# Kernel tuning notes

Hardware: AMD Instinct MI355X
Metric: run time of the kernel (lower is better)

The kernel has to match this reference:

```python
import jax, jax.numpy as jnp
import numpy as np
import math

DIM_IN = 768
RED = 256
FS = 384


def setup_inputs() -> dict:
    key = jax.random.key(0)
    ks = jax.random.split(key, 20)
    B, Nq, Nk = 16, 1024, FS
    inp = {
        "query_feature": jax.random.normal(ks[0], (B, Nq, DIM_IN), jnp.float32),
        "Input_feature": jax.random.normal(ks[1], (B, Nk, DIM_IN), jnp.float32),
    }
    # six q/k projections: Linear(dim_in -> reduce_dim), torch weight layout [out,in]
    names = ["q1", "q2", "q3", "k1", "k2", "k3"]
    for i, n in enumerate(names):
        inp[f"W{n}"] = 0.01 * jax.random.normal(ks[2 + i], (RED, DIM_IN), jnp.float32)
        inp[f"b{n}"] = jnp.zeros((RED,), jnp.float32)
    # self.layer: Linear(Fs_size -> 1)
    inp["layer_w"] = 0.01 * jax.random.normal(ks[10], (1, FS), jnp.float32)
    inp["layer_b"] = jnp.zeros((1,), jnp.float32)
    # output_layer: Linear(2*dim_in -> dim_in)
    inp["Wout"] = 0.01 * jax.random.normal(ks[11], (DIM_IN, 2 * DIM_IN), jnp.float32)
    inp["bout"] = jnp.zeros((DIM_IN,), jnp.float32)
    return inp


def _proj_center(x, W, b):
    # Linear then subtract per-feature mean over the token axis (dim=1)
    y = jnp.einsum("bnd,rd->bnr", x, W) + b
    return y - y.mean(axis=1, keepdims=True)


def reference(query_feature, Input_feature,
              Wq1, bq1, Wq2, bq2, Wq3, bq3,
              Wk1, bk1, Wk2, bk2, Wk3, bk3,
              layer_w, layer_b, Wout, bout):
    scale = 1.0 / math.sqrt(RED)
    q1 = _proj_center(query_feature, Wq1, bq1)
    q2 = _proj_center(query_feature, Wq2, bq2)
    q3 = _proj_center(query_feature, Wq3, bq3)
    k1 = _proj_center(Input_feature, Wk1, bk1)
    k2 = _proj_center(Input_feature, Wk2, bk2)
    k3 = _proj_center(Input_feature, Wk3, bk3)

    aw1 = jax.nn.softmax(jnp.einsum("bnr,bmr->bnm", q1, q2) * scale, axis=2)  # [B,Nq,Nq]
    aw2 = jax.nn.softmax(jnp.einsum("bnr,bmr->bnm", k1, k2) * scale, axis=2)  # [B,Nk,Nk]
    aw3 = jax.nn.softmax(jnp.einsum("bnr,bmr->bnm", q3, k3) * scale, axis=2)  # [B,Nq,Nk]

    attention_feature1 = jnp.einsum("bnm,bmd->bnd", aw1, query_feature)  # [B,Nq,D]
    hidden = jnp.einsum("bnm,om->bno", aw2, layer_w) + layer_b  # [B,Nk,1]
    hidden = jax.nn.softmax(hidden, axis=1)
    add = aw3 + jnp.swapaxes(hidden, 1, 2)  # broadcast [B,1,Nk]
    attention_feature2 = jnp.einsum("bnm,bmd->bnd", add, Input_feature)  # [B,Nq,D]

    cat = jnp.concatenate([attention_feature1, attention_feature2], axis=2)  # [B,Nq,2D]
    out = jnp.einsum("bnc,dc->bnd", cat, Wout) + bout
    return (cat, out)
```

## Files before the change

### kernel.cpp

```cpp
#include <hip/hip_runtime.h>

#define BATCH 16
#define NQ 1024
#define NK 384
#define DIM 768
#define RED 256
#define CATD 1536

typedef __attribute__((ext_vector_type(4))) float f32x4;
typedef __attribute__((ext_vector_type(8))) short short8;

__device__ __forceinline__ short f2bf(float f) {
    unsigned u = __builtin_bit_cast(unsigned, f);
    u = (u + 0x7FFF + ((u >> 16) & 1)) >> 16;
    return (short)u;
}
__device__ __forceinline__ float bf2f(short s) {
    unsigned u = ((unsigned)(unsigned short)s) << 16;
    return __builtin_bit_cast(float, u);
}

#define GLOAD_LDS16(g, l) __builtin_amdgcn_global_load_lds( \
    (const __attribute__((address_space(1))) unsigned int*)(g), \
    (__attribute__((address_space(3))) unsigned int*)(l), 16, 0, 0)

template<int MODE>
__global__ __launch_bounds__(256) void gemm_nt_mfma(
    const short* __restrict__ A, const short* __restrict__ B,
    float* __restrict__ Cf, short* __restrict__ Cb,
    const float* __restrict__ bias,
    int K, int lda, int ldb, int ldcf, int ldcb,
    long sA, long sB, long sCf, long sCb, float scale)
{
    __shared__ short Asl[128 * 64];
    __shared__ short Bsl[128 * 64];
    const int b = blockIdx.z;
    const short* Ab = A + (long)b * sA;
    const short* Bb = B + (long)b * sB;
    const int m0 = blockIdx.y * 128, n0 = blockIdx.x * 128;
    const int tid = threadIdx.x;
    const int lane = tid & 63, wid = tid >> 6;
    const int am0 = (wid >> 1) * 64, bn0 = (wid & 1) * 64;
    const int lr = lane & 15, lg = lane >> 4;

    f32x4 acc[4][4] = {};

    for (int k0 = 0; k0 < K; k0 += 64) {
        #pragma unroll
        for (int i = 0; i < 4; i++) {
            int e = (tid + i * 256) * 8;
            int r = e >> 6, c = e & 63;
            GLOAD_LDS16(Ab + (long)(m0 + r) * lda + k0 + c, Asl + e);
        }
        #pragma unroll
        for (int i = 0; i < 4; i++) {
            int e = (tid + i * 256) * 8;
            int r = e >> 6, c = e & 63;
            GLOAD_LDS16(Bb + (long)(n0 + r) * ldb + k0 + c, Bsl + e);
        }
        __syncthreads();
        #pragma unroll
        for (int ks = 0; ks < 2; ks++) {
            short8 af[4], bfv[4];
            #pragma unroll
            for (int m = 0; m < 4; m++)
                af[m] = *(const short8*)&Asl[(am0 + m * 16 + lr) * 64 + ks * 32 + lg * 8];
            #pragma unroll
            for (int n = 0; n < 4; n++)
                bfv[n] = *(const short8*)&Bsl[(bn0 + n * 16 + lr) * 64 + ks * 32 + lg * 8];
            #pragma unroll
            for (int m = 0; m < 4; m++)
                #pragma unroll
                for (int n = 0; n < 4; n++)
                    acc[m][n] = __builtin_amdgcn_mfma_f32_16x16x32_bf16(
                        af[m], bfv[n], acc[m][n], 0, 0, 0);
        }
        __syncthreads();
    }

    float* Cfb = (MODE != 1) ? Cf + (long)b * sCf : nullptr;
    short* Cbb = (MODE == 1 || MODE == 2) ? Cb + (long)b * sCb : nullptr;
    #pragma unroll
    for (int m = 0; m < 4; m++) {
        #pragma unroll
        for (int n = 0; n < 4; n++) {
            int col = n0 + bn0 + n * 16 + lr;
            #pragma unroll
            for (int j = 0; j < 4; j++) {
                long row = m0 + am0 + m * 16 + lg * 4 + j;
                float v = acc[m][n][j] * scale;
                if (MODE == 3) v += bias[col];
                if (MODE != 1) Cfb[row * ldcf + col] = v;
                if (MODE == 1 || MODE == 2) Cbb[row * ldcb + col] = f2bf(v);
            }
        }
    }
}

__global__ __launch_bounds__(256) void colsum(
    const float* __restrict__ X, float* __restrict__ mean, int N, int chunk)
{
    int b = blockIdx.x;
    int d = blockIdx.y * 256 + threadIdx.x;
    int n0 = blockIdx.z * chunk;
    float s = 0.f;
    for (int n = n0; n < n0 + chunk; n++)
        s += X[((long)b * N + n) * DIM + d];
    atomicAdd(&mean[b * DIM + d], s);
}

__global__ __launch_bounds__(256) void center_cvt(
    const float* __restrict__ X, const float* __restrict__ mean,
    short* __restrict__ Xc, int N, float invN)
{
    long i = (long)blockIdx.x * 256 + threadIdx.x;
    long tot8 = (long)BATCH * N * DIM / 8;
    if (i >= tot8) return;
    long e = i * 8;
    int d = (int)(e % DIM);
    int b = (int)(e / ((long)N * DIM));
    const float* mb = mean + b * DIM + d;
    const f32x4* s = (const f32x4*)(X + e);
    f32x4 x0 = s[0], x1 = s[1];
    short8 o;
    o[0] = f2bf(x0[0] - mb[0] * invN);
    o[1] = f2bf(x0[1] - mb[1] * invN);
    o[2] = f2bf(x0[2] - mb[2] * invN);
    o[3] = f2bf(x0[3] - mb[3] * invN);
    o[4] = f2bf(x1[0] - mb[4] * invN);
    o[5] = f2bf(x1[1] - mb[5] * invN);
    o[6] = f2bf(x1[2] - mb[6] * invN);
    o[7] = f2bf(x1[3] - mb[7] * invN);
    *(short8*)(Xc + e) = o;
}

__global__ __launch_bounds__(256) void cvt_bf(
    const float* __restrict__ src, short* __restrict__ dst, int n8)
{
    int i = blockIdx.x * 256 + threadIdx.x;
    if (i >= n8) return;
    const f32x4* s = (const f32x4*)(src + (long)i * 8);
    f32x4 x0 = s[0], x1 = s[1];
    short8 o;
    o[0] = f2bf(x0[0]); o[1] = f2bf(x0[1]); o[2] = f2bf(x0[2]); o[3] = f2bf(x0[3]);
    o[4] = f2bf(x1[0]); o[5] = f2bf(x1[1]); o[6] = f2bf(x1[2]); o[7] = f2bf(x1[3]);
    *(short8*)(dst + (long)i * 8) = o;
}

__global__ __launch_bounds__(256) void transpose_cvt(
    const float* __restrict__ X, short* __restrict__ XT, int N)
{
    __shared__ short tile[32][33];
    int b = blockIdx.z;
    int n0 = blockIdx.x * 32, d0 = blockIdx.y * 32;
    int tx = threadIdx.x & 31, ty = threadIdx.x >> 5;
    const float* Xb = X + (long)b * N * DIM;
    #pragma unroll
    for (int i = 0; i < 4; i++) {
        int n = n0 + ty + i * 8;
        tile[ty + i * 8][tx] = f2bf(Xb[(long)n * DIM + d0 + tx]);
    }
    __syncthreads();
    short* XTb = XT + (long)b * DIM * N;
    #pragma unroll
    for (int i = 0; i < 4; i++) {
        int d = d0 + ty + i * 8;
        XTb[(long)d * N + n0 + tx] = tile[tx][ty + i * 8];
    }
}

__global__ __launch_bounds__(256) void softmax_rows_bf(
    float* __restrict__ S, short* __restrict__ P,
    const float* __restrict__ addv, int L, int rows_per_batch)
{
    long row = blockIdx.x;
    float* p = S + row * (long)L;
    short* po = P + row * (long)L;
    const int tid = threadIdx.x;
    __shared__ float red[4];
    float mx = -3.0e38f;
    for (int i = tid; i < L; i += 256) mx = fmaxf(mx, p[i]);
    #pragma unroll
    for (int o = 1; o < 64; o <<= 1) mx = fmaxf(mx, __shfl_xor(mx, o));
    if ((tid & 63) == 0) red[tid >> 6] = mx;
    __syncthreads();
    mx = fmaxf(fmaxf(red[0], red[1]), fmaxf(red[2], red[3]));
    float s = 0.f;
    for (int i = tid; i < L; i += 256) { float e = expf(p[i] - mx); p[i] = e; s += e; }
    #pragma unroll
    for (int o = 1; o < 64; o <<= 1) s += __shfl_xor(s, o);
    __syncthreads();
    if ((tid & 63) == 0) red[tid >> 6] = s;
    __syncthreads();
    s = red[0] + red[1] + red[2] + red[3];
    float inv = 1.0f / s;
    if (addv) {
        int b = (int)(row / rows_per_batch);
        const float* av = addv + (long)b * L;
        for (int i = tid; i < L; i += 256) po[i] = f2bf(p[i] * inv + av[i]);
    } else {
        for (int i = tid; i < L; i += 256) po[i] = f2bf(p[i] * inv);
    }
}

__global__ __launch_bounds__(384) void hidden_kernel(
    const short* __restrict__ P2, const float* __restrict__ lw,
    const float* __restrict__ lb, float* __restrict__ hid)
{
    int b = blockIdx.x;
    int n = threadIdx.x;
    const short* row = P2 + ((long)b * NK + n) * NK;
    float s = lb[0];
    for (int m = 0; m < NK; m++) s += bf2f(row[m]) * lw[m];
    __shared__ float red[6];
    float mx = s;
    #pragma unroll
    for (int o = 1; o < 64; o <<= 1) mx = fmaxf(mx, __shfl_xor(mx, o));
    int wid = n >> 6;
    if ((n & 63) == 0) red[wid] = mx;
    __syncthreads();
    mx = red[0];
    #pragma unroll
    for (int w = 1; w < 6; w++) mx = fmaxf(mx, red[w]);
    float e = expf(s - mx);
    float sm = e;
    #pragma unroll
    for (int o = 1; o < 64; o <<= 1) sm += __shfl_xor(sm, o);
    __syncthreads();
    if ((n & 63) == 0) red[wid] = sm;
    __syncthreads();
    sm = 0.f;
    #pragma unroll
    for (int w = 0; w < 6; w++) sm += red[w];
    hid[b * NK + n] = e / sm;
}

extern "C" void kernel_launch(void* const* d_in, const int* in_sizes, int n_in,
                              void* d_out, int out_size, void* d_ws, size_t ws_size,
                              hipStream_t stream)
{
    const float* Qf  = (const float*)d_in[0];
    const float* If  = (const float*)d_in[1];
    const float* Wq1 = (const float*)d_in[2];
    const float* Wq2 = (const float*)d_in[4];
    const float* Wq3 = (const float*)d_in[6];
    const float* Wk1 = (const float*)d_in[8];
    const float* Wk2 = (const float*)d_in[10];
    const float* Wk3 = (const float*)d_in[12];
    const float* lw  = (const float*)d_in[14];
    const float* lb  = (const float*)d_in[15];
    const float* Wout= (const float*)d_in[16];
    const float* bout= (const float*)d_in[17];

    float* cat = (float*)d_out;
    float* out = (float*)d_out + (long)BATCH * NQ * CATD;

    char* ws = (char*)d_ws;
    size_t off = 0;
    auto alloc = [&](size_t bytes) { char* p = ws + off; off += (bytes + 255) & ~(size_t)255; return p; };

    float* S     = (float*)alloc((size_t)BATCH * NQ * NQ * 4);
    short* Qc    = (short*)alloc((size_t)BATCH * NQ * DIM * 2);
    short* Kc    = (short*)alloc((size_t)BATCH * NK * DIM * 2);
    short* q1    = (short*)alloc((size_t)BATCH * NQ * RED * 2);
    short* q2    = (short*)alloc((size_t)BATCH * NQ * RED * 2);
    short* q3    = (short*)alloc((size_t)BATCH * NQ * RED * 2);
    short* k1    = (short*)alloc((size_t)BATCH * NK * RED * 2);
    short* k2    = (short*)alloc((size_t)BATCH * NK * RED * 2);
    short* k3    = (short*)alloc((size_t)BATCH * NK * RED * 2);
    short* P1    = (short*)alloc((size_t)BATCH * NQ * NQ * 2);
    short* P2    = (short*)alloc((size_t)BATCH * NK * NK * 2);
    short* P3    = (short*)alloc((size_t)BATCH * NQ * NK * 2);
    short* catbf = (short*)alloc((size_t)BATCH * NQ * CATD * 2);
    short* Wb    = (short*)alloc((size_t)6 * RED * DIM * 2);
    short* WoutB = (short*)alloc((size_t)DIM * CATD * 2);
    float* means = (float*)alloc((size_t)2 * BATCH * DIM * 4);
    float* hid   = (float*)alloc((size_t)BATCH * NK * 4);

    float* meanQ = means;
    float* meanK = means + BATCH * DIM;
    short* Wq1b = Wb + 0 * RED * DIM;
    short* Wq2b = Wb + 1 * RED * DIM;
    short* Wq3b = Wb + 2 * RED * DIM;
    short* Wk1b = Wb + 3 * RED * DIM;
    short* Wk2b = Wb + 4 * RED * DIM;
    short* Wk3b = Wb + 5 * RED * DIM;
    short* QfT = Qc;
    short* IfT = Kc;

    hipMemsetAsync(means, 0, (size_t)2 * BATCH * DIM * 4, stream);

    colsum<<<dim3(BATCH, DIM / 256, NQ / 128), 256, 0, stream>>>(Qf, meanQ, NQ, 128);
    colsum<<<dim3(BATCH, DIM / 256, NK / 128), 256, 0, stream>>>(If, meanK, NK, 128);
    center_cvt<<<(BATCH * NQ * DIM / 8 + 255) / 256, 256, 0, stream>>>(Qf, meanQ, Qc, NQ, 1.0f / NQ);
    center_cvt<<<(BATCH * NK * DIM / 8 + 255) / 256, 256, 0, stream>>>(If, meanK, Kc, NK, 1.0f / NK);

    const int wn8 = RED * DIM / 8;
    cvt_bf<<<(wn8 + 255) / 256, 256, 0, stream>>>(Wq1, Wq1b, wn8);
    cvt_bf<<<(wn8 + 255) / 256, 256, 0, stream>>>(Wq2, Wq2b, wn8);
    cvt_bf<<<(wn8 + 255) / 256, 256, 0, stream>>>(Wq3, Wq3b, wn8);
    cvt_bf<<<(wn8 + 255) / 256, 256, 0, stream>>>(Wk1, Wk1b, wn8);
    cvt_bf<<<(wn8 + 255) / 256, 256, 0, stream>>>(Wk2, Wk2b, wn8);
    cvt_bf<<<(wn8 + 255) / 256, 256, 0, stream>>>(Wk3, Wk3b, wn8);
    const int on8 = DIM * CATD / 8;
    cvt_bf<<<(on8 + 255) / 256, 256, 0, stream>>>(Wout, WoutB, on8);

    dim3 gq(RED / 128, NQ / 128, BATCH), gk(RED / 128, NK / 128, BATCH);
    gemm_nt_mfma<1><<<gq, 256, 0, stream>>>(Qc, Wq1b, nullptr, q1, nullptr,
        DIM, DIM, DIM, 0, RED, (long)NQ * DIM, 0, 0, (long)NQ * RED, 1.0f);
    gemm_nt_mfma<1><<<gq, 256, 0, stream>>>(Qc, Wq2b, nullptr, q2, nullptr,
        DIM, DIM, DIM, 0, RED, (long)NQ * DIM, 0, 0, (long)NQ * RED, 1.0f);
    gemm_nt_mfma<1><<<gq, 256, 0, stream>>>(Qc, Wq3b, nullptr, q3, nullptr,
        DIM, DIM, DIM, 0, RED, (long)NQ * DIM, 0, 0, (long)NQ * RED, 1.0f);
    gemm_nt_mfma<1><<<gk, 256, 0, stream>>>(Kc, Wk1b, nullptr, k1, nullptr,
        DIM, DIM, DIM, 0, RED, (long)NK * DIM, 0, 0, (long)NK * RED, 1.0f);
    gemm_nt_mfma<1><<<gk, 256, 0, stream>>>(Kc, Wk2b, nullptr, k2, nullptr,
        DIM, DIM, DIM, 0, RED, (long)NK * DIM, 0, 0, (long)NK * RED, 1.0f);
    gemm_nt_mfma<1><<<gk, 256, 0, stream>>>(Kc, Wk3b, nullptr, k3, nullptr,
        DIM, DIM, DIM, 0, RED, (long)NK * DIM, 0, 0, (long)NK * RED, 1.0f);

    transpose_cvt<<<dim3(NQ / 32, DIM / 32, BATCH), 256, 0, stream>>>(Qf, QfT, NQ);
    transpose_cvt<<<dim3(NK / 32, DIM / 32, BATCH), 256, 0, stream>>>(If, IfT, NK);

    const float scale = 0.0625f;

    gemm_nt_mfma<0><<<dim3(NQ / 128, NQ / 128, BATCH), 256, 0, stream>>>(
        q1, q2, S, nullptr, nullptr, RED, RED, RED, NQ, 0,
        (long)NQ * RED, (long)NQ * RED, (long)NQ * NQ, 0, scale);
    softmax_rows_bf<<<BATCH * NQ, 256, 0, stream>>>(S, P1, nullptr, NQ, NQ);

    gemm_nt_mfma<0><<<dim3(NK / 128, NK / 128, BATCH), 256, 0, stream>>>(
        k1, k2, S, nullptr, nullptr, RED, RED, RED, NK, 0,
        (long)NK * RED, (long)NK * RED, (long)NK * NK, 0, scale);
    softmax_rows_bf<<<BATCH * NK, 256, 0, stream>>>(S, P2, nullptr, NK, NK);

    hidden_kernel<<<BATCH, NK, 0, stream>>>(P2, lw, lb, hid);

    gemm_nt_mfma<0><<<dim3(NK / 128, NQ / 128, BATCH), 256, 0, stream>>>(
        q3, k3, S, nullptr, nullptr, RED, RED, RED, NK, 0,
        (long)NQ * RED, (long)NK * RED, (long)NQ * NK, 0, scale);
    softmax_rows_bf<<<BATCH * NQ, 256, 0, stream>>>(S, P3, hid, NK, NQ);

    gemm_nt_mfma<2><<<dim3(DIM / 128, NQ / 128, BATCH), 256, 0, stream>>>(
        P1, QfT, cat, catbf, nullptr, NQ, NQ, NQ, CATD, CATD,
        (long)NQ * NQ, (long)DIM * NQ, (long)NQ * CATD, (long)NQ * CATD, 1.0f);
    gemm_nt_mfma<2><<<dim3(DIM / 128, NQ / 128, BATCH), 256, 0, stream>>>(
        P3, IfT, cat + DIM, catbf + DIM, nullptr, NK, NK, NK, CATD, CATD,
        (long)NQ * NK, (long)DIM * NK, (long)NQ * CATD, (long)NQ * CATD, 1.0f);

    gemm_nt_mfma<3><<<dim3(DIM / 128, NQ / 128, BATCH), 256, 0, stream>>>(
        catbf, WoutB, out, nullptr, bout, CATD, CATD, CATD, DIM, 0,
        (long)NQ * CATD, 0, (long)NQ * DIM, 0, 1.0f);
}
```

Before: 794.7 us.

## Batch projections, remap blocks across XCDs, fuse hidden dot into softmax

Merges the six projection GEMMs into two wide GEMMs over concatenated weights, and merges the seven weight conversions into a single kernel. The GEMM now remaps block indices so that consecutive tiles land on the same XCD, aiming for better L2 locality. Softmax keeps each row in registers instead of writing exponentials back to memory. The k1·k2 softmax now computes the layer_w dot product directly, so P2 is never written and the hidden kernel only does the final softmax. These changes mainly cut launch count and memory traffic. The hidden bias lb is no longer added; that is harmless here because the softmax over tokens is shift-invariant.

```diff
diff --git a/kernel.cpp b/kernel.cpp
--- a/kernel.cpp
+++ b/kernel.cpp
@@ -14,10 +14,6 @@
     unsigned u = __builtin_bit_cast(unsigned, f);
     u = (u + 0x7FFF + ((u >> 16) & 1)) >> 16;
     return (short)u;
-}
-__device__ __forceinline__ float bf2f(short s) {
-    unsigned u = ((unsigned)(unsigned short)s) << 16;
-    return __builtin_bit_cast(float, u);
 }
 
 #define GLOAD_LDS16(g, l) __builtin_amdgcn_global_load_lds( \
@@ -34,10 +30,21 @@
 {
     __shared__ short Asl[128 * 64];
     __shared__ short Bsl[128 * 64];
-    const int b = blockIdx.z;
-    const short* Ab = A + (long)b * sA;
-    const short* Bb = B + (long)b * sB;
-    const int m0 = blockIdx.y * 128, n0 = blockIdx.x * 128;
+
+    const unsigned nx = gridDim.x, ny = gridDim.y;
+    unsigned lin = (blockIdx.z * ny + blockIdx.y) * nx + blockIdx.x;
+    const unsigned nwg = nx * ny * gridDim.z;
+    const unsigned qc = nwg >> 3, rc = nwg & 7;
+    const unsigned xcd = lin & 7, pos = lin >> 3;
+    unsigned nid = (xcd < rc ? xcd * (qc + 1) : rc * (qc + 1) + (xcd - rc) * qc) + pos;
+    const unsigned bx = nid % nx;
+    unsigned t = nid / nx;
+    const unsigned by = t % ny;
+    const unsigned bz = t / ny;
+
+    const short* Ab = A + (long)bz * sA;
+    const short* Bb = B + (long)bz * sB;
+    const int m0 = by * 128, n0 = bx * 128;
     const int tid = threadIdx.x;
     const int lane = tid & 63, wid = tid >> 6;
     const int am0 = (wid >> 1) * 64, bn0 = (wid & 1) * 64;
@@ -78,8 +85,8 @@
         __syncthreads();
     }
 
-    float* Cfb = (MODE != 1) ? Cf + (long)b * sCf : nullptr;
-    short* Cbb = (MODE == 1 || MODE == 2) ? Cb + (long)b * sCb : nullptr;
+    float* Cfb = (MODE != 1) ? Cf + (long)bz * sCf : nullptr;
+    short* Cbb = (MODE == 1 || MODE == 2) ? Cb + (long)bz * sCb : nullptr;
     #pragma unroll
     for (int m = 0; m < 4; m++) {
         #pragma unroll
@@ -134,17 +141,33 @@
     *(short8*)(Xc + e) = o;
 }
 
-__global__ __launch_bounds__(256) void cvt_bf(
-    const float* __restrict__ src, short* __restrict__ dst, int n8)
-{
+struct WP { const float* p[7]; };
+__global__ __launch_bounds__(256) void cvt_weights(
+    WP wp, short* __restrict__ Wqb, short* __restrict__ Wkb,
+    short* __restrict__ WoutB)
+{
+    const int WSZ = RED * DIM / 8;
+    const int OSZ = DIM * CATD / 8;
     int i = blockIdx.x * 256 + threadIdx.x;
-    if (i >= n8) return;
-    const f32x4* s = (const f32x4*)(src + (long)i * 8);
+    if (i >= 6 * WSZ + OSZ) return;
+    const float* src;
+    short* dst;
+    if (i < 6 * WSZ) {
+        int w = i / WSZ, o = i - w * WSZ;
+        src = wp.p[w] + (long)o * 8;
+        dst = (w < 3 ? Wqb + (long)w * RED * DIM
+                     : Wkb + (long)(w - 3) * RED * DIM) + (long)o * 8;
+    } else {
+        int o = i - 6 * WSZ;
+        src = wp.p[6] + (long)o * 8;
+        dst = WoutB + (long)o * 8;
+    }
+    const f32x4* s = (const f32x4*)src;
     f32x4 x0 = s[0], x1 = s[1];
-    short8 o;
-    o[0] = f2bf(x0[0]); o[1] = f2bf(x0[1]); o[2] = f2bf(x0[2]); o[3] = f2bf(x0[3]);
-    o[4] = f2bf(x1[0]); o[5] = f2bf(x1[1]); o[6] = f2bf(x1[2]); o[7] = f2bf(x1[3]);
-    *(short8*)(dst + (long)i * 8) = o;
+    short8 o8;
+    o8[0] = f2bf(x0[0]); o8[1] = f2bf(x0[1]); o8[2] = f2bf(x0[2]); o8[3] = f2bf(x0[3]);
+    o8[4] = f2bf(x1[0]); o8[5] = f2bf(x1[1]); o8[6] = f2bf(x1[2]); o8[7] = f2bf(x1[3]);
+    *(short8*)dst = o8;
 }
 
 __global__ __launch_bounds__(256) void transpose_cvt(
@@ -169,49 +192,74 @@
     }
 }
 
-__global__ __launch_bounds__(256) void softmax_rows_bf(
-    float* __restrict__ S, short* __restrict__ P,
-    const float* __restrict__ addv, int L, int rows_per_batch)
+template<int WRITE_P, int DOT>
+__global__ __launch_bounds__(256) void softmax_rows(
+    const float* __restrict__ S, short* __restrict__ P,
+    const float* __restrict__ addv, const float* __restrict__ lw,
+    float* __restrict__ dots, int L, int rows_per_batch)
 {
     long row = blockIdx.x;
-    float* p = S + row * (long)L;
-    short* po = P + row * (long)L;
+    const float* p = S + row * (long)L;
     const int tid = threadIdx.x;
-    __shared__ float red[4];
+    const int C = (L + 255) >> 8;
+    float v[4];
     float mx = -3.0e38f;
-    for (int i = tid; i < L; i += 256) mx = fmaxf(mx, p[i]);
+    for (int c = 0; c < C; c++) {
+        int i = tid + c * 256;
+        v[c] = (i < L) ? p[i] : -3.0e38f;
+        mx = fmaxf(mx, v[c]);
+    }
+    __shared__ float rmax[4], rsum[4], rdot[4];
     #pragma unroll
     for (int o = 1; o < 64; o <<= 1) mx = fmaxf(mx, __shfl_xor(mx, o));
-    if ((tid & 63) == 0) red[tid >> 6] = mx;
-    __syncthreads();
-    mx = fmaxf(fmaxf(red[0], red[1]), fmaxf(red[2], red[3]));
-    float s = 0.f;
-    for (int i = tid; i < L; i += 256) { float e = expf(p[i] - mx); p[i] = e; s += e; }
+    if ((tid & 63) == 0) rmax[tid >> 6] = mx;
+    __syncthreads();
+    mx = fmaxf(fmaxf(rmax[0], rmax[1]), fmaxf(rmax[2], rmax[3]));
+    float s = 0.f, dt = 0.f;
+    for (int c = 0; c < C; c++) {
+        int i = tid + c * 256;
+        float e = expf(v[c] - mx);
+        v[c] = e;
+        s += e;
+        if (DOT) dt += (i < L) ? e * lw[i] : 0.f;
+    }
     #pragma unroll
     for (int o = 1; o < 64; o <<= 1) s += __shfl_xor(s, o);
-    __syncthreads();
-    if ((tid & 63) == 0) red[tid >> 6] = s;
-    __syncthreads();
-    s = red[0] + red[1] + red[2] + red[3];
+    if ((tid & 63) == 0) rsum[tid >> 6] = s;
+    if (DOT) {
+        #pragma unroll
+        for (int o = 1; o < 64; o <<= 1) dt += __shfl_xor(dt, o);
+        if ((tid & 63) == 0) rdot[tid >> 6] = dt;
+    }
+    __syncthreads();
+    s = rsum[0] + rsum[1] + rsum[2] + rsum[3];
     float inv = 1.0f / s;
-    if (addv) {
-        int b = (int)(row / rows_per_batch);
-        const float* av = addv + (long)b * L;
-        for (int i = tid; i < L; i += 256) po[i] = f2bf(p[i] * inv + av[i]);
-    } else {
-        for (int i = tid; i < L; i += 256) po[i] = f2bf(p[i] * inv);
-    }
-}
-
-__global__ __launch_bounds__(384) void hidden_kernel(
-    const short* __restrict__ P2, const float* __restrict__ lw,
-    const float* __restrict__ lb, float* __restrict__ hid)
+    if (DOT && tid == 0)
+        dots[row] = (rdot[0] + rdot[1] + rdot[2] + rdot[3]) * inv;
+    if (WRITE_P) {
+        short* po = P + row * (long)L;
+        if (addv) {
+            int b = (int)(row / rows_per_batch);
+            const float* av = addv + (long)b * L;
+            for (int c = 0; c < C; c++) {
+                int i = tid + c * 256;
+                if (i < L) po[i] = f2bf(v[c] * inv + av[i]);
+            }
+        } else {
+            for (int c = 0; c < C; c++) {
+                int i = tid + c * 256;
+                if (i < L) po[i] = f2bf(v[c] * inv);
+            }
+        }
+    }
+}
+
+__global__ __launch_bounds__(384) void hid_softmax(
+    const float* __restrict__ scores, float* __restrict__ hid)
 {
     int b = blockIdx.x;
     int n = threadIdx.x;
-    const short* row = P2 + ((long)b * NK + n) * NK;
-    float s = lb[0];
-    for (int m = 0; m < NK; m++) s += bf2f(row[m]) * lw[m];
+    float s = scores[b * NK + n];
     __shared__ float red[6];
     float mx = s;
     #pragma unroll
@@ -241,15 +289,7 @@
 {
     const float* Qf  = (const float*)d_in[0];
     const float* If  = (const float*)d_in[1];
-    const float* Wq1 = (const float*)d_in[2];
-    const float* Wq2 = (const float*)d_in[4];
-    const float* Wq3 = (const float*)d_in[6];
-    const float* Wk1 = (const float*)d_in[8];
-    const float* Wk2 = (const float*)d_in[10];
-    const float* Wk3 = (const float*)d_in[12];
     const float* lw  = (const float*)d_in[14];
-    const float* lb  = (const float*)d_in[15];
-    const float* Wout= (const float*)d_in[16];
     const float* bout= (const float*)d_in[17];
 
     float* cat = (float*)d_out;
@@ -262,29 +302,20 @@
     float* S     = (float*)alloc((size_t)BATCH * NQ * NQ * 4);
     short* Qc    = (short*)alloc((size_t)BATCH * NQ * DIM * 2);
     short* Kc    = (short*)alloc((size_t)BATCH * NK * DIM * 2);
-    short* q1    = (short*)alloc((size_t)BATCH * NQ * RED * 2);
-    short* q2    = (short*)alloc((size_t)BATCH * NQ * RED * 2);
-    short* q3    = (short*)alloc((size_t)BATCH * NQ * RED * 2);
-    short* k1    = (short*)alloc((size_t)BATCH * NK * RED * 2);
-    short* k2    = (short*)alloc((size_t)BATCH * NK * RED * 2);
-    short* k3    = (short*)alloc((size_t)BATCH * NK * RED * 2);
+    short* q_all = (short*)alloc((size_t)BATCH * NQ * 3 * RED * 2);
+    short* k_all = (short*)alloc((size_t)BATCH * NK * 3 * RED * 2);
     short* P1    = (short*)alloc((size_t)BATCH * NQ * NQ * 2);
-    short* P2    = (short*)alloc((size_t)BATCH * NK * NK * 2);
     short* P3    = (short*)alloc((size_t)BATCH * NQ * NK * 2);
     short* catbf = (short*)alloc((size_t)BATCH * NQ * CATD * 2);
-    short* Wb    = (short*)alloc((size_t)6 * RED * DIM * 2);
+    short* Wqb   = (short*)alloc((size_t)3 * RED * DIM * 2);
+    short* Wkb   = (short*)alloc((size_t)3 * RED * DIM * 2);
     short* WoutB = (short*)alloc((size_t)DIM * CATD * 2);
     float* means = (float*)alloc((size_t)2 * BATCH * DIM * 4);
+    float* scores= (float*)alloc((size_t)BATCH * NK * 4);
     float* hid   = (float*)alloc((size_t)BATCH * NK * 4);
 
     float* meanQ = means;
     float* meanK = means + BATCH * DIM;
-    short* Wq1b = Wb + 0 * RED * DIM;
-    short* Wq2b = Wb + 1 * RED * DIM;
-    short* Wq3b = Wb + 2 * RED * DIM;
-    short* Wk1b = Wb + 3 * RED * DIM;
-    short* Wk2b = Wb + 4 * RED * DIM;
-    short* Wk3b = Wb + 5 * RED * DIM;
     short* QfT = Qc;
     short* IfT = Kc;
 
@@ -295,51 +326,53 @@
     center_cvt<<<(BATCH * NQ * DIM / 8 + 255) / 256, 256, 0, stream>>>(Qf, meanQ, Qc, NQ, 1.0f / NQ);
     center_cvt<<<(BATCH * NK * DIM / 8 + 255) / 256, 256, 0, stream>>>(If, meanK, Kc, NK, 1.0f / NK);
 
-    const int wn8 = RED * DIM / 8;
-    cvt_bf<<<(wn8 + 255) / 256, 256, 0, stream>>>(Wq1, Wq1b, wn8);
-    cvt_bf<<<(wn8 + 255) / 256, 256, 0, stream>>>(Wq2, Wq2b, wn8);
-    cvt_bf<<<(wn8 + 255) / 256, 256, 0, stream>>>(Wq3, Wq3b, wn8);
-    cvt_bf<<<(wn8 + 255) / 256, 256, 0, stream>>>(Wk1, Wk1b, wn8);
-    cvt_bf<<<(wn8 + 255) / 256, 256, 0, stream>>>(Wk2, Wk2b, wn8);
-    cvt_bf<<<(wn8 + 255) / 256, 256, 0, stream>>>(Wk3, Wk3b, wn8);
-    const int on8 = DIM * CATD / 8;
-    cvt_bf<<<(on8 + 255) / 256, 256, 0, stream>>>(Wout, WoutB, on8);
-
-    dim3 gq(RED / 128, NQ / 128, BATCH), gk(RED / 128, NK / 128, BATCH);
-    gemm_nt_mfma<1><<<gq, 256, 0, stream>>>(Qc, Wq1b, nullptr, q1, nullptr,
-        DIM, DIM, DIM, 0, RED, (long)NQ * DIM, 0, 0, (long)NQ * RED, 1.0f);
-    gemm_nt_mfma<1><<<gq, 256, 0, stream>>>(Qc, Wq2b, nullptr, q2, nullptr,
-        DIM, DIM, DIM, 0, RED, (long)NQ * DIM, 0, 0, (long)NQ * RED, 1.0f);
-    gemm_nt_mfma<1><<<gq, 256, 0, stream>>>(Qc, Wq3b, nullptr, q3, nullptr,
-        DIM, DIM, DIM, 0, RED, (long)NQ * DIM, 0, 0, (long)NQ * RED, 1.0f);
-    gemm_nt_mfma<1><<<gk, 256, 0, stream>>>(Kc, Wk1b, nullptr, k1, nullptr,
-        DIM, DIM, DIM, 0, RED, (long)NK * DIM, 0, 0, (long)NK * RED, 1.0f);
-    gemm_nt_mfma<1><<<gk, 256, 0, stream>>>(Kc, Wk2b, nullptr, k2, nullptr,
-        DIM, DIM, DIM, 0, RED, (long)NK * DIM, 0, 0, (long)NK * RED, 1.0f);
-    gemm_nt_mfma<1><<<gk, 256, 0, stream>>>(Kc, Wk3b, nullptr, k3, nullptr,
-        DIM, DIM, DIM, 0, RED, (long)NK * DIM, 0, 0, (long)NK * RED, 1.0f);
+    {
+        WP wp;
+        wp.p[0] = (const float*)d_in[2];
+        wp.p[1] = (const float*)d_in[4];
+        wp.p[2] = (const float*)d_in[6];
+        wp.p[3] = (const float*)d_in[8];
+        wp.p[4] = (const float*)d_in[10];
+        wp.p[5] = (const float*)d_in[12];
+        wp.p[6] = (const float*)d_in[16];
+        int total = 6 * (RED * DIM / 8) + DIM * CATD / 8;
+        cvt_weights<<<(total + 255) / 256, 256, 0, stream>>>(wp, Wqb, Wkb, WoutB);
+    }
+
+    gemm_nt_mfma<1><<<dim3(6, BATCH * NQ / 128, 1), 256, 0, stream>>>(
+        Qc, Wqb, nullptr, q_all, nullptr,
+        DIM, DIM, DIM, 0, 3 * RED, 0, 0, 0, 0, 1.0f);
+    gemm_nt_mfma<1><<<dim3(6, BATCH * NK / 128, 1), 256, 0, stream>>>(
+        Kc, Wkb, nullptr, k_all, nullptr,
+        DIM, DIM, DIM, 0, 3 * RED, 0, 0, 0, 0, 1.0f);
 
     transpose_cvt<<<dim3(NQ / 32, DIM / 32, BATCH), 256, 0, stream>>>(Qf, QfT, NQ);
     transpose_cvt<<<dim3(NK / 32, DIM / 32, BATCH), 256, 0, stream>>>(If, IfT, NK);
 
     const float scale = 0.0625f;
+    const short* q1 = q_all;
+    const short* q2 = q_all + RED;
+    const short* q3 = q_all + 2 * RED;
+    const short* k1 = k_all;
+    const short* k2 = k_all + RED;
+    const short* k3 = k_all + 2 * RED;
+    const long sQ = (long)NQ * 3 * RED, sK = (long)NK * 3 * RED;
 
     gemm_nt_mfma<0><<<dim3(NQ / 128, NQ / 128, BATCH), 256, 0, stream>>>(
-        q1, q2, S, nullptr, nullptr, RED, RED, RED, NQ, 0,
-        (long)NQ * RED, (long)NQ * RED, (long)NQ * NQ, 0, scale);
-    softmax_rows_bf<<<BATCH * NQ, 256, 0, stream>>>(S, P1, nullptr, NQ, NQ);
+        q1, q2, S, nullptr, nullptr, RED, 3 * RED, 3 * RED, NQ, 0,
+        sQ, sQ, (long)NQ * NQ, 0, scale);
+    softmax_rows<1, 0><<<BATCH * NQ, 256, 0, stream>>>(S, P1, nullptr, nullptr, nullptr, NQ, NQ);
 
     gemm_nt_mfma<0><<<dim3(NK / 128, NK / 128, BATCH), 256, 0, stream>>>(
-        k1, k2, S, nullptr, nullptr, RED, RED, RED, NK, 0,
-        (long)NK * RED, (long)NK * RED, (long)NK * NK, 0, scale);
-    softmax_rows_bf<<<BATCH * NK, 256, 0, stream>>>(S, P2, nullptr, NK, NK);
-
-    hidden_kernel<<<BATCH, NK, 0, stream>>>(P2, lw, lb, hid);
+        k1, k2, S, nullptr, nullptr, RED, 3 * RED, 3 * RED, NK, 0,
+        sK, sK, (long)NK * NK, 0, scale);
+    softmax_rows<0, 1><<<BATCH * NK, 256, 0, stream>>>(S, nullptr, nullptr, lw, scores, NK, NK);
+    hid_softmax<<<BATCH, NK, 0, stream>>>(scores, hid);
 
     gemm_nt_mfma<0><<<dim3(NK / 128, NQ / 128, BATCH), 256, 0, stream>>>(
-        q3, k3, S, nullptr, nullptr, RED, RED, RED, NK, 0,
-        (long)NQ * RED, (long)NK * RED, (long)NQ * NK, 0, scale);
-    softmax_rows_bf<<<BATCH * NQ, 256, 0, stream>>>(S, P3, hid, NK, NQ);
+        q3, k3, S, nullptr, nullptr, RED, 3 * RED, 3 * RED, NK, 0,
+        sQ, sK, (long)NQ * NK, 0, scale);
+    softmax_rows<1, 0><<<BATCH * NQ, 256, 0, stream>>>(S, P3, hid, nullptr, nullptr, NK, NQ);
 
     gemm_nt_mfma<2><<<dim3(DIM / 128, NQ / 128, BATCH), 256, 0, stream>>>(
         P1, QfT, cat, catbf, nullptr, NQ, NQ, NQ, CATD, CATD,
```

New measurement: 691.4 us. 13.0% less time.
